# Performance work log

Measured on AMD Instinct MI355X. Metric: run time of the kernel, lower is better.

Reference implementation:

```python
import jax, jax.numpy as jnp
import numpy as np

EPS = 1e-3          # keras BatchNormalization default epsilon
DT = 0.2
LAM2 = 4.0          # lambda_diffusion**2 = 2.0**2
K = 5

def _bn(x, gamma, beta, mean, var):
    # inference-mode batch norm over channel (last) axis
    return (x - mean) * jax.lax.rsqrt(var + EPS) * gamma + beta

def _conv(x, w):
    # NHWC 'same' conv, stride 1, no bias
    return jax.lax.conv_general_dilated(x, w, (1, 1), 'SAME',
                                        dimension_numbers=('NHWC', 'HWIO', 'NHWC'))

def _sobel_edges(x):
    # tf.image.sobel_edges: per-channel 3x3 Sobel with REFLECT padding.
    # returns (dy, dx) matching sobel[...,0], sobel[...,1]
    p = jnp.pad(x, ((0, 0), (1, 1), (1, 1), (0, 0)), mode='reflect')
    dy = (p[:, 2:, :-2] + 2 * p[:, 2:, 1:-1] + p[:, 2:, 2:]) \
       - (p[:, :-2, :-2] + 2 * p[:, :-2, 1:-1] + p[:, :-2, 2:])
    dx = (p[:, :-2, 2:] + 2 * p[:, 1:-1, 2:] + p[:, 2:, 2:]) \
       - (p[:, :-2, :-2] + 2 * p[:, 1:-1, :-2] + p[:, 2:, :-2])
    return dy, dx

def setup_inputs() -> dict:
    key = jax.random.key(0)
    k1, k2, k3 = jax.random.split(key, 3)
    B, H, W, Cin, Cout = 16, 128, 128, 64, 64
    c = jnp.float32
    return {
        'x':   jax.random.normal(k1, (B, H, W, Cin), dtype=c),
        'f_w': jax.random.normal(k2, (3, 3, Cin, Cout), dtype=c) * 0.05,
        'g_w': jax.random.normal(k3, (3, 3, Cout, Cout), dtype=c) * 0.05,
        'bnf_gamma': jnp.ones((Cin,), c),  'bnf_beta': jnp.zeros((Cin,), c),
        'bnf_mean':  jnp.zeros((Cin,), c), 'bnf_var':  jnp.ones((Cin,), c),
        'bng_gamma': jnp.ones((Cout,), c), 'bng_beta': jnp.zeros((Cout,), c),
        'bng_mean':  jnp.zeros((Cout,), c),'bng_var':  jnp.ones((Cout,), c),
        'bno_gamma': jnp.ones((Cout,), c), 'bno_beta': jnp.zeros((Cout,), c),
        'bno_mean':  jnp.zeros((Cout,), c),'bno_var':  jnp.ones((Cout,), c),
    }

def reference(x, f_w, g_w,
              bnf_gamma, bnf_beta, bnf_mean, bnf_var,
              bng_gamma, bng_beta, bng_mean, bng_var,
              bno_gamma, bno_beta, bno_mean, bno_var):
    f = _conv(jax.nn.relu(_bn(x, bnf_gamma, bnf_beta, bnf_mean, bnf_var)), f_w)
    h = f
    g = _conv(jax.nn.relu(_bn(h, bng_gamma, bng_beta, bng_mean, bng_var)), g_w)
    g1 = g
    dy, dx = _sobel_edges(h)
    Dx = 1.0 / (dy * dy / LAM2 + 1.0)   # source: sobel[..., 0]
    Dy = 1.0 / (dx * dx / LAM2 + 1.0)   # source: sobel[..., 1]
    # NOTE: faithful to source — rolls on axis=2 (W) and axis=3 (channels in NHWC)
    ux = 0.5 * (jnp.roll(g, 1, axis=2) - jnp.roll(g, -1, axis=2))
    vy = 0.5 * (jnp.roll(g1, 1, axis=3) - jnp.roll(g1, -1, axis=3))
    Ax = g * DT
    Ay = g1 * DT
    Bx = Dx * DT
    By = Dy * DT
    E = (ux + vy) * DT
    D = 1.0 / (1.0 + 2 * Bx + 2 * By)
    h0 = h
    for _ in range(K):
        prev = h
        h = D * ((1 - 2 * Bx - 2 * By) * h0
                 - 2 * E * h
                 + (-Ax + 2 * Bx) * jnp.roll(h, 1, axis=2)
                 + ( Ax + 2 * Bx) * jnp.roll(h, -1, axis=2)
                 + (-Ay + 2 * By) * jnp.roll(h, 1, axis=3)
                 + ( Ay + 2 * By) * jnp.roll(h, -1, axis=3)
                 + 2 * DT * f)
        h0 = prev
    h = jax.nn.relu(_bn(h, bno_gamma, bno_beta, bno_mean, bno_var))
    return (h, g)
```

## Files before the change

### kernel.cpp

```cpp
#include <hip/hip_runtime.h>

#define HH 128
#define WW 128
#define CC 64
#define ROW (WW*CC)
#define PADW 72

typedef _Float16 half8 __attribute__((ext_vector_type(8)));
typedef _Float16 half4v __attribute__((ext_vector_type(4)));
typedef float floatx4 __attribute__((ext_vector_type(4)));

__global__ __launch_bounds__(256)
void repack_w(const float* __restrict__ wf, const float* __restrict__ wg,
              _Float16* __restrict__ W2f, _Float16* __restrict__ W2g)
{
    int idx = blockIdx.x * 256 + threadIdx.x;
    int sel = idx >= 36864;
    int id  = sel ? idx - 36864 : idx;
    const float* src = sel ? wg : wf;
    _Float16* dst = sel ? W2g : W2f;
    int t = id >> 12, c = (id >> 6) & 63, o = id & 63;
    int kc = c >> 5, q = (c >> 3) & 3, j = c & 7;
    int pos = ((((t*2 + kc)*4 + q)*64 + o) << 3) + j;
    dst[pos] = (_Float16)src[id];
}

template<int BNIN, int EPI>
__global__ __launch_bounds__(256, 2)
void conv_mfma(const void* __restrict__ srcv, const _Float16* __restrict__ W2,
               _Float16* __restrict__ outH, float* __restrict__ outF,
               _Float16* __restrict__ y2,
               const float* __restrict__ ig, const float* __restrict__ ib,
               const float* __restrict__ imu, const float* __restrict__ iva,
               const float* __restrict__ og, const float* __restrict__ ob,
               const float* __restrict__ om, const float* __restrict__ ov)
{
    __shared__ __align__(16) _Float16 sIn[4*130*PADW];
    const int t = threadIdx.x;
    const int blk = ((blockIdx.x & 7) << 7) | (blockIdx.x >> 3);
    const int b = blk >> 6, i0 = (blk & 63) * 2;

    const int c8 = (t & 7) << 3;
    float scv[8], biv[8];
    if (BNIN) {
        #pragma unroll
        for (int j = 0; j < 8; ++j) {
            float s = ig[c8+j] * rsqrtf(iva[c8+j] + 1e-3f);
            scv[j] = s; biv[j] = ib[c8+j] - imu[c8+j]*s;
        }
    }

    for (int r = 0; r < 4; ++r) {
        int iy = i0 - 1 + r;
        bool inb = (iy >= 0) && (iy < HH);
        #pragma unroll
        for (int k = 0; k < 4; ++k) {
            int idx = t + (k << 8);
            int px = idx >> 3;
            half8 v = {0,0,0,0,0,0,0,0};
            if (inb) {
                if (BNIN) {
                    const float* gp = (const float*)srcv
                        + ((size_t)(b*HH + iy))*ROW + px*CC + c8;
                    float4 u0 = *(const float4*)gp;
                    float4 u1 = *(const float4*)(gp + 4);
                    v[0] = (_Float16)fmaxf(0.f, u0.x*scv[0] + biv[0]);
                    v[1] = (_Float16)fmaxf(0.f, u0.y*scv[1] + biv[1]);
                    v[2] = (_Float16)fmaxf(0.f, u0.z*scv[2] + biv[2]);
                    v[3] = (_Float16)fmaxf(0.f, u0.w*scv[3] + biv[3]);
                    v[4] = (_Float16)fmaxf(0.f, u1.x*scv[4] + biv[4]);
                    v[5] = (_Float16)fmaxf(0.f, u1.y*scv[5] + biv[5]);
                    v[6] = (_Float16)fmaxf(0.f, u1.z*scv[6] + biv[6]);
                    v[7] = (_Float16)fmaxf(0.f, u1.w*scv[7] + biv[7]);
                } else {
                    v = *(const half8*)((const _Float16*)srcv
                        + ((size_t)(b*HH + iy))*ROW + px*CC + c8);
                }
            }
            *(half8*)(sIn + (r*130 + px + 1)*PADW + c8) = v;
        }
    }
    if (t < 128) {
        int rr = t >> 5, s = (t >> 4) & 1, c4 = (t & 15) << 2;
        int slot = s ? 129 : 0;
        half4v z = {0,0,0,0};
        *(half4v*)(sIn + (rr*130 + slot)*PADW + c4) = z;
    }
    __syncthreads();

    const int wv = t >> 6, lane = t & 63;
    const int lm = lane & 15, quad = lane >> 4;
    const int r  = wv >> 1;
    const int px0 = (wv & 1) * 64;
    floatx4 z4 = {0.f,0.f,0.f,0.f};
    floatx4 acc[4][4];
    #pragma unroll
    for (int ms = 0; ms < 4; ++ms)
        #pragma unroll
        for (int nt = 0; nt < 4; ++nt) acc[ms][nt] = z4;

    #pragma unroll
    for (int tap = 0; tap < 9; ++tap) {
        const int di = tap / 3, dj = tap % 3;
        #pragma unroll
        for (int kc = 0; kc < 2; ++kc) {
            const _Float16* ab = sIn + ((r + di)*130 + px0 + lm + dj)*PADW
                               + kc*32 + quad*8;
            half8 a0 = *(const half8*)(ab);
            half8 a1 = *(const half8*)(ab + 16*PADW);
            half8 a2 = *(const half8*)(ab + 32*PADW);
            half8 a3 = *(const half8*)(ab + 48*PADW);
            const _Float16* wb = W2 + (((tap*2 + kc)*4 + quad) << 9) + (lm << 3);
            half8 b0 = *(const half8*)(wb);
            half8 b1 = *(const half8*)(wb + 128);
            half8 b2 = *(const half8*)(wb + 256);
            half8 b3 = *(const half8*)(wb + 384);
            acc[0][0] = __builtin_amdgcn_mfma_f32_16x16x32_f16(a0, b0, acc[0][0], 0,0,0);
            acc[1][0] = __builtin_amdgcn_mfma_f32_16x16x32_f16(a1, b0, acc[1][0], 0,0,0);
            acc[2][0] = __builtin_amdgcn_mfma_f32_16x16x32_f16(a2, b0, acc[2][0], 0,0,0);
            acc[3][0] = __builtin_amdgcn_mfma_f32_16x16x32_f16(a3, b0, acc[3][0], 0,0,0);
            acc[0][1] = __builtin_amdgcn_mfma_f32_16x16x32_f16(a0, b1, acc[0][1], 0,0,0);
            acc[1][1] = __builtin_amdgcn_mfma_f32_16x16x32_f16(a1, b1, acc[1][1], 0,0,0);
            acc[2][1] = __builtin_amdgcn_mfma_f32_16x16x32_f16(a2, b1, acc[2][1], 0,0,0);
            acc[3][1] = __builtin_amdgcn_mfma_f32_16x16x32_f16(a3, b1, acc[3][1], 0,0,0);
            acc[0][2] = __builtin_amdgcn_mfma_f32_16x16x32_f16(a0, b2, acc[0][2], 0,0,0);
            acc[1][2] = __builtin_amdgcn_mfma_f32_16x16x32_f16(a1, b2, acc[1][2], 0,0,0);
            acc[2][2] = __builtin_amdgcn_mfma_f32_16x16x32_f16(a2, b2, acc[2][2], 0,0,0);
            acc[3][2] = __builtin_amdgcn_mfma_f32_16x16x32_f16(a3, b2, acc[3][2], 0,0,0);
            acc[0][3] = __builtin_amdgcn_mfma_f32_16x16x32_f16(a0, b3, acc[0][3], 0,0,0);
            acc[1][3] = __builtin_amdgcn_mfma_f32_16x16x32_f16(a1, b3, acc[1][3], 0,0,0);
            acc[2][3] = __builtin_amdgcn_mfma_f32_16x16x32_f16(a2, b3, acc[2][3], 0,0,0);
            acc[3][3] = __builtin_amdgcn_mfma_f32_16x16x32_f16(a3, b3, acc[3][3], 0,0,0);
        }
    }

    __syncthreads();
    float* sF = (float*)sIn;
    #pragma unroll
    for (int nt = 0; nt < 4; ++nt) {
        int c = nt*16 + lm;
        #pragma unroll
        for (int ms = 0; ms < 4; ++ms) {
            int pix = r*128 + px0 + ms*16 + quad*4;
            floatx4 v = acc[ms][nt];
            #pragma unroll
            for (int rv = 0; rv < 4; ++rv)
                sF[(pix + rv)*64 + c] = v[rv];
        }
    }
    __syncthreads();

    const size_t gbase = ((size_t)(b*HH + i0)) * ROW;
    if (EPI) {
        const int c8o = (t & 7) << 3;
        float s8[8], bb8[8];
        #pragma unroll
        for (int j = 0; j < 8; ++j) {
            float ss = og[c8o+j] * rsqrtf(ov[c8o+j] + 1e-3f);
            s8[j] = ss; bb8[j] = ob[c8o+j] - om[c8o+j]*ss;
        }
        #pragma unroll
        for (int jj = 0; jj < 8; ++jj) {
            int e = (jj*256 + t) << 3;
            floatx4 u0 = *(const floatx4*)(sF + e);
            floatx4 u1 = *(const floatx4*)(sF + e + 4);
            half8 hv, yv;
            #pragma unroll
            for (int j = 0; j < 4; ++j) {
                hv[j]   = (_Float16)u0[j];
                hv[4+j] = (_Float16)u1[j];
                yv[j]   = (_Float16)fmaxf(0.f, u0[j]*s8[j]   + bb8[j]);
                yv[4+j] = (_Float16)fmaxf(0.f, u1[j]*s8[4+j] + bb8[4+j]);
            }
            *(half8*)(outH + gbase + e) = hv;
            *(half8*)(y2   + gbase + e) = yv;
        }
    } else {
        #pragma unroll
        for (int jj = 0; jj < 16; ++jj) {
            int e = (jj*256 + t) << 2;
            *(floatx4*)(outF + gbase + e) = *(const floatx4*)(sF + e);
        }
    }
}

__global__ __launch_bounds__(1024, 2)
void diffuse(const _Float16* __restrict__ f, const float* __restrict__ g,
             float* __restrict__ out,
             const float* __restrict__ bog, const float* __restrict__ bob,
             const float* __restrict__ bom, const float* __restrict__ bov)
{
    __shared__ float B0[ROW], B1[ROW];
    const int t = threadIdx.x;
    const int rowb = ((blockIdx.x & 7) << 8) | (blockIdx.x >> 3);
    const int b = rowb >> 7, i = rowb & 127;
    const int im = (i == 0)    ? 1    : i - 1;
    const int ip = (i == HH-1) ? HH-2 : i + 1;
    const _Float16* fb  = f + (size_t)b * (HH*ROW);
    const _Float16* frm = fb + (size_t)im * ROW;
    const _Float16* fr0 = fb + (size_t)i  * ROW;
    const _Float16* frp = fb + (size_t)ip * ROW;
    const float* grow = g + (size_t)rowb * ROW;

    const int lane = t & 63;
    const int srcm = (lane & 48) | ((lane - 1) & 15);
    const int srcp = (lane & 48) | ((lane + 1) & 15);
    const int w0 = t >> 4, c0 = (t & 15) << 2;
    const int qch[2] = { t*4, t*4 + 4096 };
    const int wch[2] = { w0, w0 + 64 };

    #pragma unroll
    for (int k = 0; k < 2; ++k) {
        half4v vm = *(const half4v*)(frm + qch[k]);
        half4v vp = *(const half4v*)(frp + qch[k]);
        floatx4 a = { (float)vm[0], (float)vm[1], (float)vm[2], (float)vm[3] };
        floatx4 p = { (float)vp[0], (float)vp[1], (float)vp[2], (float)vp[3] };
        *(floatx4*)(B0 + qch[k]) = a;
        *(floatx4*)(B1 + qch[k]) = p;
    }
    __syncthreads();

    floatx4 Bx4[2], dxp4[2];
    #pragma unroll
    for (int k = 0; k < 2; ++k) {
        int w = wch[k];
        int wm = (w == 0)    ? 1      : w - 1;
        int wp = (w == WW-1) ? WW - 2 : w + 1;
        floatx4 am = *(const floatx4*)(B0 + wm*CC + c0);
        floatx4 a0 = *(const floatx4*)(B0 + w *CC + c0);
        floatx4 ap = *(const floatx4*)(B0 + wp*CC + c0);
        floatx4 bm = *(const floatx4*)(B1 + wm*CC + c0);
        floatx4 b0 = *(const floatx4*)(B1 + w *CC + c0);
        floatx4 bp = *(const floatx4*)(B1 + wp*CC + c0);
        floatx4 dy = (bm + 2.f*b0 + bp) - (am + 2.f*a0 + ap);
        Bx4[k]  = 0.2f / (dy*dy*0.25f + 1.f);
        dxp4[k] = (ap - am) + (bp - bm);
    }
    __syncthreads();

    #pragma unroll
    for (int k = 0; k < 2; ++k) {
        half4v v0 = *(const half4v*)(fr0 + qch[k]);
        floatx4 fv = { (float)v0[0], (float)v0[1], (float)v0[2], (float)v0[3] };
        *(floatx4*)(B0 + qch[k]) = fv;
        *(floatx4*)(B1 + qch[k]) = *(const floatx4*)(grow + qch[k]);
    }
    __syncthreads();

    floatx4 P4[2], R4[2], Q4[2], cH0[2], cEE[2], cF[2], h4[2], h04[2];
    #pragma unroll
    for (int k = 0; k < 2; ++k) {
        int w = wch[k];
        int wm = (w == 0)    ? 1      : w - 1;
        int wp = (w == WW-1) ? WW - 2 : w + 1;
        int wl = (w + WW - 1) & (WW - 1);
        int wr = (w + 1) & (WW - 1);
        floatx4 fm = *(const floatx4*)(B0 + wm*CC + c0);
        floatx4 fv = *(const floatx4*)(B0 + w *CC + c0);
        floatx4 fp = *(const floatx4*)(B0 + wp*CC + c0);
        floatx4 dx = dxp4[k] + 2.f*(fp - fm);
        floatx4 By = 0.2f / (dx*dx*0.25f + 1.f);
        floatx4 Bx = Bx4[k];
        floatx4 gv = *(const floatx4*)(B1 + w *CC + c0);
        floatx4 gl = *(const floatx4*)(B1 + wl*CC + c0);
        floatx4 gr = *(const floatx4*)(B1 + wr*CC + c0);
        float gdm = __shfl(gv[3], srcm, 64);
        float gup = __shfl(gv[0], srcp, 64);
        floatx4 gd = { gdm, gv[0], gv[1], gv[2] };
        floatx4 gu = { gv[1], gv[2], gv[3], gup };
        floatx4 E  = ((gl - gr) + (gd - gu)) * 0.1f;
        floatx4 A  = gv * 0.2f;
        floatx4 Dd = 1.f / (1.f + 2.f*Bx + 2.f*By);
        cH0[k] = 2.f*Dd - 1.f;
        cEE[k] = -2.f * E * Dd;
        P4[k]  = 2.f * Bx * Dd;
        R4[k]  = 2.f * By * Dd;
        Q4[k]  = A * Dd;
        cF[k]  = 0.4f * Dd * fv;
        h4[k] = fv; h04[k] = fv;
    }
    __syncthreads();

    int oWl[2], oWr[2];
    #pragma unroll
    for (int k = 0; k < 2; ++k) {
        int w = wch[k];
        oWl[k] = ((w + WW - 1) & (WW - 1))*CC + c0;
        oWr[k] = ((w + 1) & (WW - 1))*CC + c0;
    }

    float* cur = B0;
    float* oth = B1;
    for (int it = 0; it < 5; ++it) {
        #pragma unroll
        for (int k = 0; k < 2; ++k) {
            floatx4 hl = *(const floatx4*)(cur + oWl[k]);
            floatx4 hr = *(const floatx4*)(cur + oWr[k]);
            floatx4 hv = h4[k];
            float hdm = __shfl(hv[3], srcm, 64);
            float hup = __shfl(hv[0], srcp, 64);
            floatx4 hd = { hdm, hv[0], hv[1], hv[2] };
            floatx4 hu = { hv[1], hv[2], hv[3], hup };
            floatx4 hn = cH0[k]*h04[k] + cEE[k]*hv
                       + P4[k]*(hl + hr) + R4[k]*(hd + hu)
                       + Q4[k]*((hr - hl) + (hu - hd)) + cF[k];
            *(floatx4*)(oth + qch[k]) = hn;
            h04[k] = hv; h4[k] = hn;
        }
        __syncthreads();
        float* tmp = cur; cur = oth; oth = tmp;
    }

    floatx4 gg = *(const floatx4*)(bog + c0);
    floatx4 vv = *(const floatx4*)(bov + c0);
    floatx4 bb = *(const floatx4*)(bob + c0);
    floatx4 mm = *(const floatx4*)(bom + c0);
    floatx4 s4, bi4;
    #pragma unroll
    for (int j = 0; j < 4; ++j) s4[j] = gg[j] * rsqrtf(vv[j] + 1e-3f);
    bi4 = bb - mm*s4;
    float* op = out + (size_t)rowb * ROW;
    #pragma unroll
    for (int k = 0; k < 2; ++k) {
        floatx4 rr = h4[k]*s4 + bi4;
        #pragma unroll
        for (int j = 0; j < 4; ++j) rr[j] = fmaxf(0.f, rr[j]);
        *(floatx4*)(op + qch[k]) = rr;
    }
}

extern "C" void kernel_launch(void* const* d_in, const int* in_sizes, int n_in,
                              void* d_out, int out_size, void* d_ws, size_t ws_size,
                              hipStream_t stream)
{
    const float* x    = (const float*)d_in[0];
    const float* f_w  = (const float*)d_in[1];
    const float* g_w  = (const float*)d_in[2];
    const float* bnf_g = (const float*)d_in[3];
    const float* bnf_b = (const float*)d_in[4];
    const float* bnf_m = (const float*)d_in[5];
    const float* bnf_v = (const float*)d_in[6];
    const float* bng_g = (const float*)d_in[7];
    const float* bng_b = (const float*)d_in[8];
    const float* bng_m = (const float*)d_in[9];
    const float* bng_v = (const float*)d_in[10];
    const float* bno_g = (const float*)d_in[11];
    const float* bno_b = (const float*)d_in[12];
    const float* bno_m = (const float*)d_in[13];
    const float* bno_v = (const float*)d_in[14];

    float* out = (float*)d_out;
    const size_t N = (size_t)16 * HH * WW * CC;
    _Float16* y2   = (_Float16*)d_ws;
    _Float16* fbuf = y2 + N;
    _Float16* W2f  = y2 + 2*N;
    _Float16* W2g  = W2f + 36864;

    repack_w<<<288, 256, 0, stream>>>(f_w, g_w, W2f, W2g);
    conv_mfma<1,1><<<1024, 256, 0, stream>>>(x, W2f, fbuf, nullptr, y2,
                                             bnf_g, bnf_b, bnf_m, bnf_v,
                                             bng_g, bng_b, bng_m, bng_v);
    conv_mfma<0,0><<<1024, 256, 0, stream>>>(y2, W2g, nullptr, out + N, nullptr,
                                             nullptr, nullptr, nullptr, nullptr,
                                             nullptr, nullptr, nullptr, nullptr);
    diffuse<<<2048, 1024, 0, stream>>>(fbuf, out + N, out, bno_g, bno_b, bno_m, bno_v);
}
```

Measured before the change: 344.1 us.

## Rework diffuse kernel: 8 channels per thread, padded LDS rows, folded coefficients

The diffuse kernel is restructured so each thread handles 8 contiguous channels of one pixel instead of two 4-channel chunks. LDS rows are padded to a stride of 66 floats, intended to reduce bank conflicts. All global loads for f and g are issued up front. The stencil coefficients are pre-combined (P±Q, R±Q) so the inner update becomes a chain of six FMAs, and divisions use the fast hardware reciprocal. The occupancy hint in launch_bounds is dropped and the iteration loop is fully unrolled, which raises register pressure and slightly changes numerics through the approximate rcp.

Result: slower. 414.9 us (+20.6%).

```diff
diff --git a/kernel.cpp b/kernel.cpp
--- a/kernel.cpp
+++ b/kernel.cpp
@@ -5,6 +5,7 @@
 #define CC 64
 #define ROW (WW*CC)
 #define PADW 72
+#define LSTR 66
 
 typedef _Float16 half8 __attribute__((ext_vector_type(8)));
 typedef _Float16 half4v __attribute__((ext_vector_type(4)));
@@ -184,149 +185,193 @@
     }
 }
 
-__global__ __launch_bounds__(1024, 2)
+__global__ __launch_bounds__(1024)
 void diffuse(const _Float16* __restrict__ f, const float* __restrict__ g,
              float* __restrict__ out,
              const float* __restrict__ bog, const float* __restrict__ bob,
              const float* __restrict__ bom, const float* __restrict__ bov)
 {
-    __shared__ float B0[ROW], B1[ROW];
+    __shared__ float B0[128*LSTR], B1[128*LSTR];
     const int t = threadIdx.x;
     const int rowb = ((blockIdx.x & 7) << 8) | (blockIdx.x >> 3);
     const int b = rowb >> 7, i = rowb & 127;
     const int im = (i == 0)    ? 1    : i - 1;
     const int ip = (i == HH-1) ? HH-2 : i + 1;
-    const _Float16* fb  = f + (size_t)b * (HH*ROW);
-    const _Float16* frm = fb + (size_t)im * ROW;
-    const _Float16* fr0 = fb + (size_t)i  * ROW;
-    const _Float16* frp = fb + (size_t)ip * ROW;
+    const _Float16* fb = f + (size_t)b * (HH*ROW);
+    const int e0 = t << 3;
+    const int w  = t >> 3;
+    const int c0 = (t & 7) << 3;
+    const int lo = w*LSTR + c0;
+    const int lane = t & 63;
+    const int srcm = (lane & 56) | ((lane - 1) & 7);
+    const int srcp = (lane & 56) | ((lane + 1) & 7);
+
+    half8 vm = *(const half8*)(fb + (size_t)im*ROW + e0);
+    half8 vp = *(const half8*)(fb + (size_t)ip*ROW + e0);
+    half8 v0 = *(const half8*)(fb + (size_t)i *ROW + e0);
     const float* grow = g + (size_t)rowb * ROW;
-
-    const int lane = t & 63;
-    const int srcm = (lane & 48) | ((lane - 1) & 15);
-    const int srcp = (lane & 48) | ((lane + 1) & 15);
-    const int w0 = t >> 4, c0 = (t & 15) << 2;
-    const int qch[2] = { t*4, t*4 + 4096 };
-    const int wch[2] = { w0, w0 + 64 };
-
-    #pragma unroll
-    for (int k = 0; k < 2; ++k) {
-        half4v vm = *(const half4v*)(frm + qch[k]);
-        half4v vp = *(const half4v*)(frp + qch[k]);
-        floatx4 a = { (float)vm[0], (float)vm[1], (float)vm[2], (float)vm[3] };
-        floatx4 p = { (float)vp[0], (float)vp[1], (float)vp[2], (float)vp[3] };
-        *(floatx4*)(B0 + qch[k]) = a;
-        *(floatx4*)(B1 + qch[k]) = p;
-    }
-    __syncthreads();
-
-    floatx4 Bx4[2], dxp4[2];
-    #pragma unroll
-    for (int k = 0; k < 2; ++k) {
-        int w = wch[k];
-        int wm = (w == 0)    ? 1      : w - 1;
-        int wp = (w == WW-1) ? WW - 2 : w + 1;
-        floatx4 am = *(const floatx4*)(B0 + wm*CC + c0);
-        floatx4 a0 = *(const floatx4*)(B0 + w *CC + c0);
-        floatx4 ap = *(const floatx4*)(B0 + wp*CC + c0);
-        floatx4 bm = *(const floatx4*)(B1 + wm*CC + c0);
-        floatx4 b0 = *(const floatx4*)(B1 + w *CC + c0);
-        floatx4 bp = *(const floatx4*)(B1 + wp*CC + c0);
-        floatx4 dy = (bm + 2.f*b0 + bp) - (am + 2.f*a0 + ap);
-        Bx4[k]  = 0.2f / (dy*dy*0.25f + 1.f);
-        dxp4[k] = (ap - am) + (bp - bm);
-    }
-    __syncthreads();
-
-    #pragma unroll
-    for (int k = 0; k < 2; ++k) {
-        half4v v0 = *(const half4v*)(fr0 + qch[k]);
-        floatx4 fv = { (float)v0[0], (float)v0[1], (float)v0[2], (float)v0[3] };
-        *(floatx4*)(B0 + qch[k]) = fv;
-        *(floatx4*)(B1 + qch[k]) = *(const floatx4*)(grow + qch[k]);
-    }
-    __syncthreads();
-
-    floatx4 P4[2], R4[2], Q4[2], cH0[2], cEE[2], cF[2], h4[2], h04[2];
-    #pragma unroll
-    for (int k = 0; k < 2; ++k) {
-        int w = wch[k];
-        int wm = (w == 0)    ? 1      : w - 1;
-        int wp = (w == WW-1) ? WW - 2 : w + 1;
-        int wl = (w + WW - 1) & (WW - 1);
-        int wr = (w + 1) & (WW - 1);
-        floatx4 fm = *(const floatx4*)(B0 + wm*CC + c0);
-        floatx4 fv = *(const floatx4*)(B0 + w *CC + c0);
-        floatx4 fp = *(const floatx4*)(B0 + wp*CC + c0);
-        floatx4 dx = dxp4[k] + 2.f*(fp - fm);
-        floatx4 By = 0.2f / (dx*dx*0.25f + 1.f);
-        floatx4 Bx = Bx4[k];
-        floatx4 gv = *(const floatx4*)(B1 + w *CC + c0);
-        floatx4 gl = *(const floatx4*)(B1 + wl*CC + c0);
-        floatx4 gr = *(const floatx4*)(B1 + wr*CC + c0);
-        float gdm = __shfl(gv[3], srcm, 64);
-        float gup = __shfl(gv[0], srcp, 64);
-        floatx4 gd = { gdm, gv[0], gv[1], gv[2] };
-        floatx4 gu = { gv[1], gv[2], gv[3], gup };
-        floatx4 E  = ((gl - gr) + (gd - gu)) * 0.1f;
-        floatx4 A  = gv * 0.2f;
-        floatx4 Dd = 1.f / (1.f + 2.f*Bx + 2.f*By);
-        cH0[k] = 2.f*Dd - 1.f;
-        cEE[k] = -2.f * E * Dd;
-        P4[k]  = 2.f * Bx * Dd;
-        R4[k]  = 2.f * By * Dd;
-        Q4[k]  = A * Dd;
-        cF[k]  = 0.4f * Dd * fv;
-        h4[k] = fv; h04[k] = fv;
-    }
-    __syncthreads();
-
-    int oWl[2], oWr[2];
-    #pragma unroll
-    for (int k = 0; k < 2; ++k) {
-        int w = wch[k];
-        oWl[k] = ((w + WW - 1) & (WW - 1))*CC + c0;
-        oWr[k] = ((w + 1) & (WW - 1))*CC + c0;
-    }
+    floatx4 g0 = *(const floatx4*)(grow + e0);
+    floatx4 g1 = *(const floatx4*)(grow + e0 + 4);
+
+    float a0f[8], b0f[8];
+    #pragma unroll
+    for (int j = 0; j < 8; ++j) { a0f[j] = (float)vm[j]; b0f[j] = (float)vp[j]; }
+    {
+        floatx4 u0 = {a0f[0],a0f[1],a0f[2],a0f[3]}, u1 = {a0f[4],a0f[5],a0f[6],a0f[7]};
+        floatx4 p0 = {b0f[0],b0f[1],b0f[2],b0f[3]}, p1 = {b0f[4],b0f[5],b0f[6],b0f[7]};
+        *(floatx4*)(B0 + lo) = u0;  *(floatx4*)(B0 + lo + 4) = u1;
+        *(floatx4*)(B1 + lo) = p0;  *(floatx4*)(B1 + lo + 4) = p1;
+    }
+    __syncthreads();
+
+    const int wm = (w == 0)    ? 1      : w - 1;
+    const int wp = (w == WW-1) ? WW - 2 : w + 1;
+    float Bx[8], dxp[8];
+    {
+        float am[8], ap[8], bm[8], bp[8];
+        floatx4 u0, u1;
+        u0 = *(const floatx4*)(B0 + wm*LSTR + c0); u1 = *(const floatx4*)(B0 + wm*LSTR + c0 + 4);
+        #pragma unroll
+        for (int j = 0; j < 4; ++j) { am[j] = u0[j]; am[4+j] = u1[j]; }
+        u0 = *(const floatx4*)(B0 + wp*LSTR + c0); u1 = *(const floatx4*)(B0 + wp*LSTR + c0 + 4);
+        #pragma unroll
+        for (int j = 0; j < 4; ++j) { ap[j] = u0[j]; ap[4+j] = u1[j]; }
+        u0 = *(const floatx4*)(B1 + wm*LSTR + c0); u1 = *(const floatx4*)(B1 + wm*LSTR + c0 + 4);
+        #pragma unroll
+        for (int j = 0; j < 4; ++j) { bm[j] = u0[j]; bm[4+j] = u1[j]; }
+        u0 = *(const floatx4*)(B1 + wp*LSTR + c0); u1 = *(const floatx4*)(B1 + wp*LSTR + c0 + 4);
+        #pragma unroll
+        for (int j = 0; j < 4; ++j) { bp[j] = u0[j]; bp[4+j] = u1[j]; }
+        #pragma unroll
+        for (int j = 0; j < 8; ++j) {
+            float dy = (bm[j] + 2.f*b0f[j] + bp[j]) - (am[j] + 2.f*a0f[j] + ap[j]);
+            Bx[j]  = 0.2f * __builtin_amdgcn_rcpf(dy*dy*0.25f + 1.f);
+            dxp[j] = (ap[j] - am[j]) + (bp[j] - bm[j]);
+        }
+    }
+    __syncthreads();
+
+    float fvr[8], gfv[8];
+    #pragma unroll
+    for (int j = 0; j < 8; ++j) fvr[j] = (float)v0[j];
+    #pragma unroll
+    for (int j = 0; j < 4; ++j) { gfv[j] = g0[j]; gfv[4+j] = g1[j]; }
+    {
+        floatx4 u0 = {fvr[0],fvr[1],fvr[2],fvr[3]}, u1 = {fvr[4],fvr[5],fvr[6],fvr[7]};
+        *(floatx4*)(B0 + lo) = u0;  *(floatx4*)(B0 + lo + 4) = u1;
+        *(floatx4*)(B1 + lo) = g0;  *(floatx4*)(B1 + lo + 4) = g1;
+    }
+    __syncthreads();
+
+    const int owl = ((w + WW - 1) & (WW - 1))*LSTR + c0;
+    const int owr = ((w + 1) & (WW - 1))*LSTR + c0;
+    float cH0[8], cEE[8], cR[8], cL[8], cU[8], cD[8], cF[8], h[8], h0v[8];
+    {
+        float fm[8], fp[8], gl[8], gr[8];
+        floatx4 u0, u1;
+        u0 = *(const floatx4*)(B0 + wm*LSTR + c0); u1 = *(const floatx4*)(B0 + wm*LSTR + c0 + 4);
+        #pragma unroll
+        for (int j = 0; j < 4; ++j) { fm[j] = u0[j]; fm[4+j] = u1[j]; }
+        u0 = *(const floatx4*)(B0 + wp*LSTR + c0); u1 = *(const floatx4*)(B0 + wp*LSTR + c0 + 4);
+        #pragma unroll
+        for (int j = 0; j < 4; ++j) { fp[j] = u0[j]; fp[4+j] = u1[j]; }
+        u0 = *(const floatx4*)(B1 + owl);          u1 = *(const floatx4*)(B1 + owl + 4);
+        #pragma unroll
+        for (int j = 0; j < 4; ++j) { gl[j] = u0[j]; gl[4+j] = u1[j]; }
+        u0 = *(const floatx4*)(B1 + owr);          u1 = *(const floatx4*)(B1 + owr + 4);
+        #pragma unroll
+        for (int j = 0; j < 4; ++j) { gr[j] = u0[j]; gr[4+j] = u1[j]; }
+        float gdm = __shfl(gfv[7], srcm, 64);
+        float gup = __shfl(gfv[0], srcp, 64);
+        float gd[8], gu[8];
+        gd[0] = gdm;
+        #pragma unroll
+        for (int j = 1; j < 8; ++j) gd[j] = gfv[j-1];
+        #pragma unroll
+        for (int j = 0; j < 7; ++j) gu[j] = gfv[j+1];
+        gu[7] = gup;
+        #pragma unroll
+        for (int j = 0; j < 8; ++j) {
+            float dx = dxp[j] + 2.f*(fp[j] - fm[j]);
+            float By = 0.2f * __builtin_amdgcn_rcpf(dx*dx*0.25f + 1.f);
+            float E  = ((gl[j] - gr[j]) + (gd[j] - gu[j])) * 0.1f;
+            float Q  = gfv[j] * 0.2f;
+            float Dd = __builtin_amdgcn_rcpf(1.f + 2.f*Bx[j] + 2.f*By);
+            float P  = 2.f*Bx[j]*Dd;
+            float R  = 2.f*By*Dd;
+            Q *= Dd;
+            cH0[j] = 2.f*Dd - 1.f;
+            cEE[j] = -2.f*E*Dd;
+            cR[j] = P + Q;  cL[j] = P - Q;
+            cU[j] = R + Q;  cD[j] = R - Q;
+            cF[j] = 0.4f*Dd*fvr[j];
+            h[j] = fvr[j];  h0v[j] = fvr[j];
+        }
+    }
+    __syncthreads();
 
     float* cur = B0;
     float* oth = B1;
+    #pragma unroll
     for (int it = 0; it < 5; ++it) {
-        #pragma unroll
-        for (int k = 0; k < 2; ++k) {
-            floatx4 hl = *(const floatx4*)(cur + oWl[k]);
-            floatx4 hr = *(const floatx4*)(cur + oWr[k]);
-            floatx4 hv = h4[k];
-            float hdm = __shfl(hv[3], srcm, 64);
-            float hup = __shfl(hv[0], srcp, 64);
-            floatx4 hd = { hdm, hv[0], hv[1], hv[2] };
-            floatx4 hu = { hv[1], hv[2], hv[3], hup };
-            floatx4 hn = cH0[k]*h04[k] + cEE[k]*hv
-                       + P4[k]*(hl + hr) + R4[k]*(hd + hu)
-                       + Q4[k]*((hr - hl) + (hu - hd)) + cF[k];
-            *(floatx4*)(oth + qch[k]) = hn;
-            h04[k] = hv; h4[k] = hn;
-        }
+        float hl[8], hr[8], hn[8];
+        floatx4 u0, u1;
+        u0 = *(const floatx4*)(cur + owl); u1 = *(const floatx4*)(cur + owl + 4);
+        #pragma unroll
+        for (int j = 0; j < 4; ++j) { hl[j] = u0[j]; hl[4+j] = u1[j]; }
+        u0 = *(const floatx4*)(cur + owr); u1 = *(const floatx4*)(cur + owr + 4);
+        #pragma unroll
+        for (int j = 0; j < 4; ++j) { hr[j] = u0[j]; hr[4+j] = u1[j]; }
+        float hdm = __shfl(h[7], srcm, 64);
+        float hup = __shfl(h[0], srcp, 64);
+        float hd[8], hu[8];
+        hd[0] = hdm;
+        #pragma unroll
+        for (int j = 1; j < 8; ++j) hd[j] = h[j-1];
+        #pragma unroll
+        for (int j = 0; j < 7; ++j) hu[j] = h[j+1];
+        hu[7] = hup;
+        #pragma unroll
+        for (int j = 0; j < 8; ++j) {
+            float a = fmaf(cH0[j], h0v[j], cF[j]);
+            a = fmaf(cEE[j], h[j],  a);
+            a = fmaf(cR[j],  hr[j], a);
+            a = fmaf(cL[j],  hl[j], a);
+            a = fmaf(cU[j],  hu[j], a);
+            a = fmaf(cD[j],  hd[j], a);
+            hn[j] = a;
+        }
+        floatx4 w0 = {hn[0],hn[1],hn[2],hn[3]}, w1 = {hn[4],hn[5],hn[6],hn[7]};
+        *(floatx4*)(oth + lo) = w0;  *(floatx4*)(oth + lo + 4) = w1;
+        #pragma unroll
+        for (int j = 0; j < 8; ++j) { h0v[j] = h[j]; h[j] = hn[j]; }
         __syncthreads();
         float* tmp = cur; cur = oth; oth = tmp;
     }
 
-    floatx4 gg = *(const floatx4*)(bog + c0);
-    floatx4 vv = *(const floatx4*)(bov + c0);
-    floatx4 bb = *(const floatx4*)(bob + c0);
-    floatx4 mm = *(const floatx4*)(bom + c0);
-    floatx4 s4, bi4;
-    #pragma unroll
-    for (int j = 0; j < 4; ++j) s4[j] = gg[j] * rsqrtf(vv[j] + 1e-3f);
-    bi4 = bb - mm*s4;
-    float* op = out + (size_t)rowb * ROW;
-    #pragma unroll
-    for (int k = 0; k < 2; ++k) {
-        floatx4 rr = h4[k]*s4 + bi4;
-        #pragma unroll
-        for (int j = 0; j < 4; ++j) rr[j] = fmaxf(0.f, rr[j]);
-        *(floatx4*)(op + qch[k]) = rr;
-    }
+    float s8[8], bi8[8];
+    {
+        floatx4 gg0 = *(const floatx4*)(bog + c0), gg1 = *(const floatx4*)(bog + c0 + 4);
+        floatx4 vv0 = *(const floatx4*)(bov + c0), vv1 = *(const floatx4*)(bov + c0 + 4);
+        floatx4 bb0 = *(const floatx4*)(bob + c0), bb1 = *(const floatx4*)(bob + c0 + 4);
+        floatx4 mm0 = *(const floatx4*)(bom + c0), mm1 = *(const floatx4*)(bom + c0 + 4);
+        #pragma unroll
+        for (int j = 0; j < 4; ++j) {
+            s8[j]   = gg0[j] * rsqrtf(vv0[j] + 1e-3f);
+            s8[4+j] = gg1[j] * rsqrtf(vv1[j] + 1e-3f);
+            bi8[j]   = bb0[j] - mm0[j]*s8[j];
+            bi8[4+j] = bb1[j] - mm1[j]*s8[4+j];
+        }
+    }
+    float* op = out + (size_t)rowb * ROW + e0;
+    floatx4 r0, r1;
+    #pragma unroll
+    for (int j = 0; j < 4; ++j) {
+        r0[j] = fmaxf(0.f, fmaf(h[j],   s8[j],   bi8[j]));
+        r1[j] = fmaxf(0.f, fmaf(h[4+j], s8[4+j], bi8[4+j]));
+    }
+    *(floatx4*)(op)     = r0;
+    *(floatx4*)(op + 4) = r1;
 }
 
 extern "C" void kernel_launch(void* const* d_in, const int* in_sizes, int n_in,
```
